# Kernel optimization log

Hardware: AMD Instinct MI355X
Metric: run time of the kernel (lower is better)

The kernel has to match this reference:

```python
import jax, jax.numpy as jnp
import numpy as np

SEQ_LEN = 4_194_304  # number of tokens
INPUT_BITS = 16      # bits per token, MSB first


def setup_inputs() -> dict:
    key = jax.random.key(0)
    # bits in {0,1}; float32 carrier (values exact, matches uint8 bit semantics)
    tokens = jax.random.randint(key, (SEQ_LEN, INPUT_BITS), 0, 2).astype(jnp.float32)
    return {"tokens": tokens}


def reference(tokens):
    # tokens: [seq_len, input_bits], MSB first, entries in {0,1}
    bits = tokens.shape[1]
    # _bits_to_int: val = val*2 + b  ==  dot with [2^(bits-1), ..., 2, 1]
    pow2 = jnp.exp2(jnp.arange(bits - 1, -1, -1, dtype=jnp.float32))  # [bits]
    values = tokens @ pow2  # [seq_len], exact for bits <= 24
    # stable ascending sort == Python list.sort on (value, original_index)
    order = jnp.argsort(values, stable=True)  # [seq_len]
    return tokens[order]  # gather rows by rank
```

## Files before the change

kernel.cpp:

```cpp
#include <hip/hip_runtime.h>
#include <stdint.h>

static constexpr uint32_t SEQN = 4194304u;
static constexpr uint32_t BINS = 65536u;
static constexpr uint32_t QWORDS = BINS / 4u;
static constexpr uint32_t NBLK = 512u;
static constexpr uint32_t NTHR = 1024u;
static constexpr uint32_t ROWS_PER_BLK = SEQN / NBLK;
static constexpr uint32_t NSEG = 8u;

__global__ __launch_bounds__(NTHR) void k_hist_lds(const float4* __restrict__ in4,
                                                   uint32_t* __restrict__ partial) {
  __shared__ uint32_t h[QWORDS];
  uint32_t tid = threadIdx.x, blk = blockIdx.x;
  uint4* hv = (uint4*)h;
  for (uint32_t i = tid; i < QWORDS / 4u; i += NTHR) hv[i] = make_uint4(0u, 0u, 0u, 0u);
  __syncthreads();
  uint32_t q = tid & 3u;
  uint32_t shift = 12u - (q << 2);
  bool leader = (q == 0u);
  const float4* base = in4 + (size_t)blk * (ROWS_PER_BLK * 4u);
#pragma unroll 4
  for (uint32_t t = 0; t < (ROWS_PER_BLK * 4u) / NTHR; ++t) {
    float4 v = base[(size_t)t * NTHR + tid];
    float nf = ((v.x * 2.0f + v.y) * 2.0f + v.z) * 2.0f + v.w;
    uint32_t part = ((uint32_t)nf) << shift;
    part += __shfl_xor(part, 1, 64);
    part += __shfl_xor(part, 2, 64);
    if (leader) atomicAdd(&h[part >> 2], 1u << ((part & 3u) << 3));
  }
  __syncthreads();
  uint4* dst = (uint4*)(partial + (size_t)blk * QWORDS);
  for (uint32_t i = tid; i < QWORDS / 4u; i += NTHR) dst[i] = hv[i];
}

__global__ __launch_bounds__(256) void k_reduceA(const uint32_t* __restrict__ partial,
                                                 uint2* __restrict__ seg) {
  uint32_t tid = threadIdx.x, blk = blockIdx.x;
  uint32_t s = blk >> 6, wg = blk & 63u;
  uint32_t w = wg * 256u + tid;
  uint32_t acc_e = 0u, acc_o = 0u;
  uint32_t p0 = s * (NBLK / NSEG);
#pragma unroll 8
  for (uint32_t p = p0; p < p0 + NBLK / NSEG; ++p) {
    uint32_t v = partial[(size_t)p * QWORDS + w];
    acc_e += v & 0x00FF00FFu;
    acc_o += (v >> 8) & 0x00FF00FFu;
  }
  seg[(size_t)s * QWORDS + w] = make_uint2(acc_e, acc_o);
}

__global__ __launch_bounds__(256) void k_scanA(const uint2* __restrict__ seg,
                                               uint32_t* __restrict__ hist,
                                               uint32_t* __restrict__ blkTot) {
  uint32_t tid = threadIdx.x, blk = blockIdx.x;
  uint32_t w = blk * 256u + tid;
  uint32_t e = 0u, o = 0u;
#pragma unroll
  for (uint32_t s = 0; s < NSEG; ++s) {
    uint2 v = seg[(size_t)s * QWORDS + w];
    e += v.x;
    o += v.y;
  }
  uint32_t c0 = e & 0xFFFFu, c2 = e >> 16, c1 = o & 0xFFFFu, c3 = o >> 16;
  ((uint4*)hist)[w] = make_uint4(c0, c1, c2, c3);
  uint32_t ssum = c0 + c1 + c2 + c3;
  for (int d = 1; d < 64; d <<= 1) ssum += __shfl_xor(ssum, d, 64);
  __shared__ uint32_t wt[4];
  if ((tid & 63u) == 0u) wt[tid >> 6] = ssum;
  __syncthreads();
  if (tid == 0u) blkTot[blk] = wt[0] + wt[1] + wt[2] + wt[3];
}

__global__ __launch_bounds__(256) void k_zero(uint32_t* __restrict__ hist) {
  uint32_t i = blockIdx.x * 256u + threadIdx.x;
  if (i < BINS) hist[i] = 0u;
}

__global__ __launch_bounds__(256) void k_hist(const float4* __restrict__ in4,
                                              uint32_t* __restrict__ hist) {
  uint32_t r = blockIdx.x * 256u + threadIdx.x;
  if (r >= SEQN) return;
  uint32_t key = 0u;
#pragma unroll
  for (uint32_t qq = 0; qq < 4u; ++qq) {
    float4 v = in4[(size_t)r * 4u + qq];
    uint32_t nib = ((uint32_t)v.x << 3) | ((uint32_t)v.y << 2) |
                   ((uint32_t)v.z << 1) | (uint32_t)v.w;
    key = (key << 4) | nib;
  }
  atomicAdd(&hist[key], 1u);
}

__global__ __launch_bounds__(256) void k_scan1(const uint32_t* __restrict__ hist,
                                               uint32_t* __restrict__ blkTot) {
  uint32_t tid = threadIdx.x, blk = blockIdx.x;
  uint32_t b0 = blk * 1024u + tid * 4u;
  uint32_t s = hist[b0] + hist[b0 + 1] + hist[b0 + 2] + hist[b0 + 3];
  for (int d = 1; d < 64; d <<= 1) s += __shfl_xor(s, d, 64);
  __shared__ uint32_t wt[4];
  if ((tid & 63u) == 0u) wt[tid >> 6] = s;
  __syncthreads();
  if (tid == 0u) blkTot[blk] = wt[0] + wt[1] + wt[2] + wt[3];
}

__global__ __launch_bounds__(256) void k_scanB(const uint32_t* __restrict__ hist,
                                               const uint32_t* __restrict__ blkTot,
                                               uint32_t* __restrict__ offs) {
  __shared__ uint32_t s_base;
  __shared__ uint32_t wt[4];
  uint32_t tid = threadIdx.x, blk = blockIdx.x;
  if (tid < 64u) {
    uint32_t v = blkTot[tid];
    uint32_t incl = v;
    for (int d = 1; d < 64; d <<= 1) {
      uint32_t n = __shfl_up(incl, d, 64);
      if (tid >= (uint32_t)d) incl += n;
    }
    if (tid == blk) s_base = incl - v;
  }
  __syncthreads();
  uint32_t lane = tid & 63u, wid = tid >> 6;
  uint32_t b0 = blk * 1024u + tid * 4u;
  uint4 c = ((const uint4*)hist)[b0 >> 2];
  uint32_t s = c.x + c.y + c.z + c.w;
  uint32_t incl = s;
  for (int d = 1; d < 64; d <<= 1) {
    uint32_t n = __shfl_up(incl, d, 64);
    if (lane >= (uint32_t)d) incl += n;
  }
  if (lane == 63u) wt[wid] = incl;
  __syncthreads();
  uint32_t wbase = 0u;
  for (uint32_t w = 0; w < wid; ++w) wbase += wt[w];
  uint32_t base = s_base + wbase + (incl - s);
  ((uint4*)offs)[b0 >> 2] = make_uint4(base, base + c.x, base + c.x + c.y,
                                       base + c.x + c.y + c.z);
}

__global__ __launch_bounds__(256) void k_write(const uint32_t* __restrict__ hist,
                                               const uint32_t* __restrict__ offs,
                                               float4* __restrict__ out4) {
  __shared__ uint32_t s_off[32], s_cnt[32];
  uint32_t tid = threadIdx.x, blk = blockIdx.x;
  if (tid < 32u) {
    uint32_t k = blk * 32u + tid;
    s_off[tid] = offs[k];
    s_cnt[tid] = hist[k];
  }
  __syncthreads();
  uint32_t q = tid & 3u;
  for (uint32_t kk = 0; kk < 32u; ++kk) {
    uint32_t k = blk * 32u + kk;
    uint32_t off = s_off[kk], cnt = s_cnt[kk];
    float4 pat;
    pat.x = (float)((k >> (15u - (q * 4u + 0u))) & 1u);
    pat.y = (float)((k >> (15u - (q * 4u + 1u))) & 1u);
    pat.z = (float)((k >> (15u - (q * 4u + 2u))) & 1u);
    pat.w = (float)((k >> (15u - (q * 4u + 3u))) & 1u);
    size_t base = (size_t)off * 4u;
    uint32_t tot = cnt * 4u;
    for (uint32_t j = tid; j < tot; j += 256u) out4[base + j] = pat;
  }
}

extern "C" void kernel_launch(void* const* d_in, const int* in_sizes, int n_in,
                              void* d_out, int out_size, void* d_ws, size_t ws_size,
                              hipStream_t stream) {
  const float4* in4 = (const float4*)d_in[0];
  float4* out4 = (float4*)d_out;
  uint32_t* hist = (uint32_t*)d_ws;
  uint32_t* offs = hist + BINS;
  uint32_t* blkTot = offs + BINS;
  uint32_t* partial = blkTot + 1024u;
  uint2* seg = (uint2*)(partial + (size_t)NBLK * QWORDS);

  size_t need = ((size_t)2 * BINS + 1024u + (size_t)NBLK * QWORDS +
                 (size_t)NSEG * QWORDS * 2u) * 4u;
  if (ws_size >= need) {
    k_hist_lds<<<NBLK, NTHR, 0, stream>>>(in4, partial);
    k_reduceA<<<NSEG * 64, 256, 0, stream>>>(partial, seg);
    k_scanA<<<64, 256, 0, stream>>>(seg, hist, blkTot);
  } else {
    k_zero<<<BINS / 256, 256, 0, stream>>>(hist);
    k_hist<<<SEQN / 256, 256, 0, stream>>>(in4, hist);
    k_scan1<<<64, 256, 0, stream>>>(hist, blkTot);
  }
  k_scanB<<<64, 256, 0, stream>>>(hist, blkTot, offs);
  k_write<<<BINS / 32, 256, 0, stream>>>(hist, offs, out4);
}
```

Baseline: 146.9 us.

## Fuse partial-histogram reduction and block totals, give each wavefront its own bins in write

Merges the two-stage partial-histogram reduction (segment sums, then scan totals) into one 64-block kernel that reduces all 512 partials through LDS. This removes a launch and the intermediate segment buffer round trip, at the cost of only 64 blocks reading the 32 MB of partials. The write kernel now gives each wavefront 8 bins instead of having the whole block walk all 32 bins, which removes idle threads on small bins. The histogram loop unroll also goes from 4 to 8.

```diff
diff --git a/kernel.cpp b/kernel.cpp
--- a/kernel.cpp
+++ b/kernel.cpp
@@ -7,7 +7,6 @@
 static constexpr uint32_t NBLK = 512u;
 static constexpr uint32_t NTHR = 1024u;
 static constexpr uint32_t ROWS_PER_BLK = SEQN / NBLK;
-static constexpr uint32_t NSEG = 8u;
 
 __global__ __launch_bounds__(NTHR) void k_hist_lds(const float4* __restrict__ in4,
                                                    uint32_t* __restrict__ partial) {
@@ -20,7 +19,7 @@
   uint32_t shift = 12u - (q << 2);
   bool leader = (q == 0u);
   const float4* base = in4 + (size_t)blk * (ROWS_PER_BLK * 4u);
-#pragma unroll 4
+#pragma unroll 8
   for (uint32_t t = 0; t < (ROWS_PER_BLK * 4u) / NTHR; ++t) {
     float4 v = base[(size_t)t * NTHR + tid];
     float nf = ((v.x * 2.0f + v.y) * 2.0f + v.z) * 2.0f + v.w;
@@ -34,40 +33,34 @@
   for (uint32_t i = tid; i < QWORDS / 4u; i += NTHR) dst[i] = hv[i];
 }
 
-__global__ __launch_bounds__(256) void k_reduceA(const uint32_t* __restrict__ partial,
-                                                 uint2* __restrict__ seg) {
+__global__ __launch_bounds__(NTHR) void k_reduceB(const uint32_t* __restrict__ partial,
+                                                  uint32_t* __restrict__ hist,
+                                                  uint32_t* __restrict__ blkTot) {
+  __shared__ uint2 acc[4][256];
+  __shared__ uint32_t wt[4];
   uint32_t tid = threadIdx.x, blk = blockIdx.x;
-  uint32_t s = blk >> 6, wg = blk & 63u;
-  uint32_t w = wg * 256u + tid;
-  uint32_t acc_e = 0u, acc_o = 0u;
-  uint32_t p0 = s * (NBLK / NSEG);
+  uint32_t wl = tid & 255u, g = tid >> 8;
+  uint32_t w = blk * 256u + wl;
+  uint32_t e = 0u, o = 0u;
+  uint32_t p0 = g * (NBLK / 4u);
 #pragma unroll 8
-  for (uint32_t p = p0; p < p0 + NBLK / NSEG; ++p) {
+  for (uint32_t p = p0; p < p0 + NBLK / 4u; ++p) {
     uint32_t v = partial[(size_t)p * QWORDS + w];
-    acc_e += v & 0x00FF00FFu;
-    acc_o += (v >> 8) & 0x00FF00FFu;
+    e += v & 0x00FF00FFu;
+    o += (v >> 8) & 0x00FF00FFu;
   }
-  seg[(size_t)s * QWORDS + w] = make_uint2(acc_e, acc_o);
-}
-
-__global__ __launch_bounds__(256) void k_scanA(const uint2* __restrict__ seg,
-                                               uint32_t* __restrict__ hist,
-                                               uint32_t* __restrict__ blkTot) {
-  uint32_t tid = threadIdx.x, blk = blockIdx.x;
-  uint32_t w = blk * 256u + tid;
-  uint32_t e = 0u, o = 0u;
-#pragma unroll
-  for (uint32_t s = 0; s < NSEG; ++s) {
-    uint2 v = seg[(size_t)s * QWORDS + w];
-    e += v.x;
-    o += v.y;
+  acc[g][wl] = make_uint2(e, o);
+  __syncthreads();
+  if (g == 0u) {
+    uint2 a1 = acc[1][wl], a2 = acc[2][wl], a3 = acc[3][wl];
+    e += a1.x + a2.x + a3.x;
+    o += a1.y + a2.y + a3.y;
+    uint32_t c0 = e & 0xFFFFu, c2 = e >> 16, c1 = o & 0xFFFFu, c3 = o >> 16;
+    ((uint4*)hist)[w] = make_uint4(c0, c1, c2, c3);
+    uint32_t ssum = c0 + c1 + c2 + c3;
+    for (int d = 1; d < 64; d <<= 1) ssum += __shfl_xor(ssum, d, 64);
+    if ((tid & 63u) == 0u) wt[tid >> 6] = ssum;
   }
-  uint32_t c0 = e & 0xFFFFu, c2 = e >> 16, c1 = o & 0xFFFFu, c3 = o >> 16;
-  ((uint4*)hist)[w] = make_uint4(c0, c1, c2, c3);
-  uint32_t ssum = c0 + c1 + c2 + c3;
-  for (int d = 1; d < 64; d <<= 1) ssum += __shfl_xor(ssum, d, 64);
-  __shared__ uint32_t wt[4];
-  if ((tid & 63u) == 0u) wt[tid >> 6] = ssum;
   __syncthreads();
   if (tid == 0u) blkTot[blk] = wt[0] + wt[1] + wt[2] + wt[3];
 }
@@ -149,10 +142,12 @@
     s_cnt[tid] = hist[k];
   }
   __syncthreads();
-  uint32_t q = tid & 3u;
-  for (uint32_t kk = 0; kk < 32u; ++kk) {
-    uint32_t k = blk * 32u + kk;
-    uint32_t off = s_off[kk], cnt = s_cnt[kk];
+  uint32_t lane = tid & 63u, wid = tid >> 6;
+  uint32_t q = lane & 3u;
+  for (uint32_t kk = 0; kk < 8u; ++kk) {
+    uint32_t ki = wid * 8u + kk;
+    uint32_t k = blk * 32u + ki;
+    uint32_t off = s_off[ki], cnt = s_cnt[ki];
     float4 pat;
     pat.x = (float)((k >> (15u - (q * 4u + 0u))) & 1u);
     pat.y = (float)((k >> (15u - (q * 4u + 1u))) & 1u);
@@ -160,7 +155,7 @@
     pat.w = (float)((k >> (15u - (q * 4u + 3u))) & 1u);
     size_t base = (size_t)off * 4u;
     uint32_t tot = cnt * 4u;
-    for (uint32_t j = tid; j < tot; j += 256u) out4[base + j] = pat;
+    for (uint32_t j = lane; j < tot; j += 64u) out4[base + j] = pat;
   }
 }
 
@@ -173,14 +168,11 @@
   uint32_t* offs = hist + BINS;
   uint32_t* blkTot = offs + BINS;
   uint32_t* partial = blkTot + 1024u;
-  uint2* seg = (uint2*)(partial + (size_t)NBLK * QWORDS);
 
-  size_t need = ((size_t)2 * BINS + 1024u + (size_t)NBLK * QWORDS +
-                 (size_t)NSEG * QWORDS * 2u) * 4u;
+  size_t need = ((size_t)2 * BINS + 1024u + (size_t)NBLK * QWORDS) * 4u;
   if (ws_size >= need) {
     k_hist_lds<<<NBLK, NTHR, 0, stream>>>(in4, partial);
-    k_reduceA<<<NSEG * 64, 256, 0, stream>>>(partial, seg);
-    k_scanA<<<64, 256, 0, stream>>>(seg, hist, blkTot);
+    k_reduceB<<<64, NTHR, 0, stream>>>(partial, hist, blkTot);
   } else {
     k_zero<<<BINS / 256, 256, 0, stream>>>(hist);
     k_hist<<<SEQN / 256, 256, 0, stream>>>(in4, hist);
```

Result: faster. 143.2 us (-2.5%).
